# Kernel optimization log

Hardware: AMD Instinct MI355X
Metric: run time of the kernel (lower is better)

The kernel has to match this reference:

```python
import jax, jax.numpy as jnp
import numpy as np

N, E, F, R, L, B = 50000, 800000, 64, 20, 2, 64
RC = 5.0
ZMAX = 100
LN2 = 0.6931471805599453

def ssp(x):
    # shifted softplus: softplus(x) - log(2)
    return jax.nn.softplus(x) - LN2

def setup_inputs() -> dict:
    key = jax.random.key(0)
    ks = jax.random.split(key, 32)
    w = lambda i, shape: jax.random.normal(ks[i], shape, dtype=jnp.float32) * 0.05
    inp = {
        'z': jax.random.randint(ks[0], (N,), 0, ZMAX + 1),
        'pos': jax.random.normal(ks[1], (N, 3), dtype=jnp.float32) * 3.0,
        'edge_index': jax.random.randint(ks[2], (2, E), 0, N),
        'batch_idx': jnp.sort(jax.random.randint(ks[3], (N,), 0, B)),
        'emb': jax.random.normal(ks[4], (ZMAX + 1, F), dtype=jnp.float32),
        'phi_W': w(5, (L, 3 * F, F)), 'phi_b': w(6, (L, 3 * F)),
        'filt_W1': w(7, (L, F, R)), 'filt_b1': w(8, (L, F)),
        'filt_W2': w(9, (L, 3 * F, F)), 'filt_b2': w(10, (L, 3 * F)),
        'U_W': w(11, (L, F, F)), 'V_W': w(12, (L, F, F)),
        'a_W1': w(13, (L, F, 2 * F)), 'a_b1': w(14, (L, F)),
        'a_W2': w(15, (L, 3 * F, F)), 'a_b2': w(16, (L, 3 * F)),
        'e_W1': w(17, (F // 2, F)), 'e_b1': w(18, (F // 2,)),
        'e_W2': w(19, (1, F // 2)), 'e_b2': w(20, (1,)),
        'dip_w': w(21, (F,)),
    }
    return inp

def reference(z, pos, edge_index, batch_idx, emb, phi_W, phi_b,
              filt_W1, filt_b1, filt_W2, filt_b2, U_W, V_W,
              a_W1, a_b1, a_W2, a_b2, e_W1, e_b1, e_W2, e_b2, dip_w):
    src, dst = edge_index[0], edge_index[1]
    s = emb[z]                               # (N, F)
    v = jnp.zeros((N, F, 3), dtype=s.dtype)  # (N, F, 3)

    # edge geometry
    r_vec = pos[dst] - pos[src]              # (E, 3)
    r_norm = jnp.linalg.norm(r_vec, axis=-1)
    r_hat = r_vec / jnp.maximum(r_norm, 1e-8)[:, None]
    # Gaussian RBF on [0, RC], widths = grid spacing
    mu = jnp.linspace(0.0, RC, R, dtype=s.dtype)
    width = mu[1] - mu[0]
    e_ij = jnp.exp(-((r_norm[:, None] - mu[None, :]) ** 2) / (2.0 * width * width))
    fc = 0.5 * (jnp.cos(jnp.pi * r_norm / RC) + 1.0) * (r_norm < RC)
    e_ij = e_ij * fc[:, None]                # (E, R)

    for l in range(L):
        # message block
        filt = ssp(e_ij @ filt_W1[l].T + filt_b1[l]) @ filt_W2[l].T + filt_b2[l]  # (E, 3F)
        W_s, W_v, W_r = jnp.split(filt, 3, axis=-1)
        phi = s[dst] @ phi_W[l].T + phi_b[l]                                       # (E, 3F)
        phi_s, phi_v, phi_r = jnp.split(phi, 3, axis=-1)
        m_s = W_s * phi_s                                                          # (E, F)
        m_v = W_v[:, :, None] * v[dst] + (W_r * phi_r)[:, :, None] * r_hat[:, None, :]  # (E, F, 3)
        s = s + jax.ops.segment_sum(m_s, src, num_segments=N)
        v = v + jax.ops.segment_sum(m_v, src, num_segments=N)
        # update block
        Uv = jnp.einsum('nfd,gf->ngd', v, U_W[l])
        Vv = jnp.einsum('nfd,gf->ngd', v, V_W[l])
        Vv_norm_sq = jnp.sum(Vv * Vv, axis=-1)                                     # (N, F)
        a = ssp(jnp.concatenate([s, Vv_norm_sq], axis=-1) @ a_W1[l].T + a_b1[l]) @ a_W2[l].T + a_b2[l]
        a_ss, a_sv, a_vv = jnp.split(a, 3, axis=-1)
        inner = jnp.sum(Uv * Vv, axis=-1)
        s = s + a_ss + a_sv * inner
        v = v + a_vv[:, :, None] * Uv

    # heads
    eps_i = (ssp(s @ e_W1.T + e_b1) @ e_W2.T + e_b2)[:, 0]  # (N,)
    energy = jax.ops.segment_sum(eps_i, batch_idx, num_segments=B)
    mu_i = jnp.sum(v * dip_w[None, :, None], axis=1)         # (N, 3)
    mu_mol = jax.ops.segment_sum(mu_i, batch_idx, num_segments=B)
    dipole = jnp.linalg.norm(mu_mol, axis=-1)
    charges = jnp.zeros((N,), dtype=s.dtype)
    return energy, dipole, charges
```

## Files before the change

### kernel.cpp

```cpp
#include <hip/hip_runtime.h>
#include <math.h>

static constexpr int N  = 50000;
static constexpr int E  = 800000;
static constexpr int F  = 64;
static constexpr int R  = 20;
static constexpr int NL = 2;
static constexpr int B  = 64;
static constexpr float RC   = 5.0f;
static constexpr float LN2F = 0.6931471805599453f;
static constexpr float WIDTH  = RC / (R - 1);
static constexpr float INV2W2 = 1.0f / (2.0f * WIDTH * WIDTH);
static constexpr float PI_F = 3.14159265358979323846f;

static constexpr int   NB     = 4096;
static constexpr float DR     = RC / NB;
static constexpr float INV_DR = NB / RC;
static constexpr int   TROWS  = NB + 2;
static constexpr int   TENT   = NB + 1;

static constexpr int NBLK_SCAN = (N + 255) / 256;

typedef __attribute__((ext_vector_type(8))) short bf16x8;
typedef __attribute__((ext_vector_type(4))) float f32x4;

__device__ __forceinline__ float ssp_f(float x) {
    return fmaxf(x, 0.0f) + log1pf(__expf(-fabsf(x))) - LN2F;
}

__device__ __forceinline__ short f2bf(float x) {
    unsigned u = __builtin_bit_cast(unsigned, x);
    unsigned r = (u + 0x7fffu + ((u >> 16) & 1u)) >> 16;
    return (short)r;
}
__device__ __forceinline__ float bf_lo(unsigned u) {
    return __builtin_bit_cast(float, u << 16);
}
__device__ __forceinline__ float bf_hi(unsigned u) {
    return __builtin_bit_cast(float, u & 0xffff0000u);
}

__global__ void k_hist(const int* __restrict__ ei, int* __restrict__ cnt) {
    int e = blockIdx.x * blockDim.x + threadIdx.x;
    if (e < E) atomicAdd(&cnt[ei[e]], 1);
}

__global__ void k_scan_a(const int* __restrict__ cnt, int* __restrict__ bsum) {
    __shared__ int part[256];
    const int t = threadIdx.x;
    const int idx = blockIdx.x * 256 + t;
    int v = (idx < N) ? cnt[idx] : 0;
    part[t] = v;
    __syncthreads();
    for (int d = 1; d < 256; d <<= 1) {
        int x = (t >= d) ? part[t - d] : 0;
        __syncthreads();
        part[t] += x;
        __syncthreads();
    }
    if (t == 255) bsum[blockIdx.x] = part[255];
}

__global__ void k_scan_b(const int* __restrict__ bsum, int* __restrict__ bpre,
                         int* __restrict__ offN) {
    __shared__ int part[256];
    const int t = threadIdx.x;
    int v = (t < NBLK_SCAN) ? bsum[t] : 0;
    part[t] = v;
    __syncthreads();
    for (int d = 1; d < 256; d <<= 1) {
        int x = (t >= d) ? part[t - d] : 0;
        __syncthreads();
        part[t] += x;
        __syncthreads();
    }
    if (t < NBLK_SCAN) bpre[t] = part[t] - v;
    if (t == NBLK_SCAN - 1) *offN = part[t];
}

__global__ void k_scan_c(const int* __restrict__ cnt, const int* __restrict__ bpre,
                         int* __restrict__ off, int* __restrict__ cur) {
    __shared__ int part[256];
    const int t = threadIdx.x;
    const int idx = blockIdx.x * 256 + t;
    int v = (idx < N) ? cnt[idx] : 0;
    part[t] = v;
    __syncthreads();
    for (int d = 1; d < 256; d <<= 1) {
        int x = (t >= d) ? part[t - d] : 0;
        __syncthreads();
        part[t] += x;
        __syncthreads();
    }
    if (idx < N) {
        int e = bpre[blockIdx.x] + part[t] - v;
        off[idx] = e;
        cur[idx] = e;
    }
}

__global__ void k_scatter(const int* __restrict__ ei, int* __restrict__ cur,
                          const float* __restrict__ pos, uint4* __restrict__ edata) {
    int e = blockIdx.x * blockDim.x + threadIdx.x;
    if (e >= E) return;
    int src = ei[e], dst = ei[E + e];
    int p = atomicAdd(&cur[src], 1);
    float qx = pos[dst * 3 + 0] - pos[src * 3 + 0];
    float qy = pos[dst * 3 + 1] - pos[src * 3 + 1];
    float qz = pos[dst * 3 + 2] - pos[src * 3 + 2];
    float rn = sqrtf(qx * qx + qy * qy + qz * qz);
    float invn = 1.0f / fmaxf(rn, 1e-8f);
    float t = rn * INV_DR;
    int i = (int)t;
    float fr = t - (float)i;
    if (i >= NB) { i = NB; fr = 0.0f; }
    uint4 rec;
    rec.x = (unsigned)dst;
    rec.y = (unsigned)i | ((unsigned)(unsigned short)f2bf(fr) << 16);
    rec.z = (unsigned)(unsigned short)f2bf(qx * invn)
          | ((unsigned)(unsigned short)f2bf(qy * invn) << 16);
    rec.w = (unsigned)(unsigned short)f2bf(qz * invn);
    edata[p] = rec;
}

__global__ void k_table(const float* __restrict__ fW1, const float* __restrict__ fb1,
                        const float* __restrict__ fW2, const float* __restrict__ fb2,
                        unsigned short* __restrict__ Tp) {
    const int l   = blockIdx.x / TROWS;
    const int row = blockIdx.x % TROWS;
    const int lane = threadIdx.x;
    const float r = fminf((float)row, (float)NB) * DR;
    const float fc = (r < RC) ? 0.5f * (__cosf(PI_F * r * (1.0f / RC)) + 1.0f) : 0.0f;

    __shared__ float sh[F];
    float acc = fb1[l * F + lane];
    const float* w1 = fW1 + (size_t)l * F * R + (size_t)lane * R;
    #pragma unroll
    for (int rr = 0; rr < R; rr++) {
        float dmu = r - rr * WIDTH;
        float er = __expf(-dmu * dmu * INV2W2) * fc;
        acc = fmaf(er, w1[rr], acc);
    }
    sh[lane] = ssp_f(acc);
    __syncthreads();
    unsigned short* TpL = Tp + (size_t)l * TENT * 384;
    #pragma unroll
    for (int p = 0; p < 3; p++) {
        int c = p * 64 + lane;
        float a = fb2[l * 192 + c];
        const float* w2 = fW2 + ((size_t)l * 192 + c) * 64;
        #pragma unroll 8
        for (int k = 0; k < F; k++) a = fmaf(sh[k], w2[k], a);
        unsigned short bf = (unsigned short)f2bf(a);
        if (row <= NB) TpL[(size_t)row * 384 + c * 2 + 0] = bf;
        if (row >= 1)  TpL[(size_t)(row - 1) * 384 + c * 2 + 1] = bf;
    }
}

template<bool HASV>
__launch_bounds__(256)
__global__ void k_pack(float* __restrict__ s, const float* __restrict__ v,
                       const int* __restrict__ z, const float* __restrict__ emb,
                       const float* __restrict__ PW, const float* __restrict__ Pb,
                       unsigned short* __restrict__ nd) {
    __shared__ float sbuf[4][F];
    const int lane = threadIdx.x & 63;
    const int wid  = threadIdx.x >> 6;
    const int gwave = blockIdx.x * 4 + wid;
    const int nwaves = gridDim.x * 4;

    float ws[F], wr[F];
    {
        const float* rs = PW + (size_t)lane * 64;
        const float* rr = PW + (size_t)(128 + lane) * 64;
        #pragma unroll
        for (int k = 0; k < F; k += 4) {
            float4 a = *(const float4*)(rs + k);
            ws[k] = a.x; ws[k+1] = a.y; ws[k+2] = a.z; ws[k+3] = a.w;
            float4 b = *(const float4*)(rr + k);
            wr[k] = b.x; wr[k+1] = b.y; wr[k+2] = b.z; wr[k+3] = b.w;
        }
    }
    const float bs = Pb[lane], br = Pb[128 + lane];

    for (int n = gwave; n < N; n += nwaves) {
        float sv;
        if (HASV) {
            sv = s[(size_t)n * F + lane];
        } else {
            sv = emb[(size_t)z[n] * F + lane];
            s[(size_t)n * F + lane] = sv;
        }
        sbuf[wid][lane] = sv;
        float as = bs, ar = br;
        #pragma unroll
        for (int k = 0; k < F; k += 4) {
            float4 s4 = *(const float4*)&sbuf[wid][k];
            as = fmaf(s4.x, ws[k],   as); as = fmaf(s4.y, ws[k+1], as);
            as = fmaf(s4.z, ws[k+2], as); as = fmaf(s4.w, ws[k+3], as);
            ar = fmaf(s4.x, wr[k],   ar); ar = fmaf(s4.y, wr[k+1], ar);
            ar = fmaf(s4.z, wr[k+2], ar); ar = fmaf(s4.w, wr[k+3], ar);
        }
        unsigned short* rec = nd + (size_t)n * 320;
        rec[lane]      = (unsigned short)f2bf(as);
        rec[64 + lane] = (unsigned short)f2bf(ar);
        if (HASV) {
            #pragma unroll
            for (int d = 0; d < 3; d++)
                rec[128 + d * 64 + lane] =
                    (unsigned short)f2bf(v[((size_t)n * 3 + d) * F + lane]);
        }
    }
}

template<bool ACCUMV>
__launch_bounds__(256)
__global__ void k_gather(const uint4* __restrict__ edata, const int* __restrict__ off,
                         const unsigned short* __restrict__ TpL,
                         const unsigned short* __restrict__ nd,
                         float* __restrict__ s, float* __restrict__ v) {
    const int lane = threadIdx.x & 63;
    const int wid  = threadIdx.x >> 6;
    const int n = blockIdx.x * 4 + wid;
    if (n >= N) return;
    const int base = off[n], end = off[n + 1];
    float ms = 0.f, mv0 = 0.f, mv1 = 0.f, mv2 = 0.f;

    for (int k = base; k < end; ++k) {
        const uint4 ed = edata[k];
        const int dst = (int)ed.x;
        const int   i  = (int)(ed.y & 0xffffu);
        const float fr = bf_hi(ed.y);
        const float rhx = bf_lo(ed.z), rhy = bf_hi(ed.z), rhz = bf_lo(ed.w);

        const unsigned* tp = (const unsigned*)(TpL + (size_t)i * 384);
        const unsigned us = tp[lane];
        const unsigned ur = tp[128 + lane];
        const float Ws = fmaf(fr, bf_hi(us) - bf_lo(us), bf_lo(us));
        const float Wr = fmaf(fr, bf_hi(ur) - bf_lo(ur), bf_lo(ur));

        const unsigned short* rec = nd + (size_t)dst * 320;
        const float ps = bf_lo((unsigned)rec[lane]);
        const float pr = bf_lo((unsigned)rec[64 + lane]);
        ms = fmaf(Ws, ps, ms);
        const float c = Wr * pr;
        if (ACCUMV) {
            const unsigned uv = tp[64 + lane];
            const float Wv = fmaf(fr, bf_hi(uv) - bf_lo(uv), bf_lo(uv));
            const float v0 = bf_lo((unsigned)rec[128 + lane]);
            const float v1 = bf_lo((unsigned)rec[192 + lane]);
            const float v2 = bf_lo((unsigned)rec[256 + lane]);
            mv0 = fmaf(Wv, v0, fmaf(c, rhx, mv0));
            mv1 = fmaf(Wv, v1, fmaf(c, rhy, mv1));
            mv2 = fmaf(Wv, v2, fmaf(c, rhz, mv2));
        } else {
            mv0 = fmaf(c, rhx, mv0);
            mv1 = fmaf(c, rhy, mv1);
            mv2 = fmaf(c, rhz, mv2);
        }
    }
    s[(size_t)n * F + lane] += ms;
    float* vo = v + (size_t)n * 3 * F + lane;
    if (ACCUMV) {
        vo[0]     += mv0;
        vo[F]     += mv1;
        vo[2 * F] += mv2;
    } else {
        vo[0] = mv0; vo[F] = mv1; vo[2 * F] = mv2;
    }
}

__device__ __forceinline__ bf16x8 load_wfrag(const float* __restrict__ Wp, int ldk,
                                             int nrow, int k0) {
    const float* p = Wp + (size_t)nrow * ldk + k0;
    float4 a = *(const float4*)p;
    float4 b = *(const float4*)(p + 4);
    bf16x8 r;
    r[0] = f2bf(a.x); r[1] = f2bf(a.y); r[2] = f2bf(a.z); r[3] = f2bf(a.w);
    r[4] = f2bf(b.x); r[5] = f2bf(b.y); r[6] = f2bf(b.z); r[7] = f2bf(b.w);
    return r;
}

__launch_bounds__(256)
__global__ void k_update_mfma(float* __restrict__ s, float* __restrict__ v,
                              const float* __restrict__ U_W, const float* __restrict__ V_W,
                              const float* __restrict__ aW1, const float* __restrict__ ab1,
                              const float* __restrict__ aW2, const float* __restrict__ ab2) {
    __shared__ short vlds[96 * 72];
    __shared__ short xlds[32 * 136];
    __shared__ short hlds[32 * 72];

    const int tid = threadIdx.x;
    const int l   = tid & 63;
    const int w   = tid >> 6;
    const int lo  = l & 15;
    const int hi  = l >> 4;

    bf16x8 ufr[2], vfr[2], w1fr[4], w2fr[3][2];
    #pragma unroll
    for (int kk = 0; kk < 2; kk++) {
        ufr[kk] = load_wfrag(U_W, 64, w * 16 + lo, kk * 32 + hi * 8);
        vfr[kk] = load_wfrag(V_W, 64, w * 16 + lo, kk * 32 + hi * 8);
    }
    #pragma unroll
    for (int kk = 0; kk < 4; kk++)
        w1fr[kk] = load_wfrag(aW1, 128, w * 16 + lo, kk * 32 + hi * 8);
    #pragma unroll
    for (int p = 0; p < 3; p++)
        #pragma unroll
        for (int kk = 0; kk < 2; kk++)
            w2fr[p][kk] = load_wfrag(aW2, 64, p * 64 + w * 16 + lo, kk * 32 + hi * 8);

    const float ab1c  = ab1[w * 16 + lo];
    const float ab2c0 = ab2[w * 16 + lo];
    const float ab2c1 = ab2[64 + w * 16 + lo];
    const float ab2c2 = ab2[128 + w * 16 + lo];
    const int g = w * 16 + lo;

    for (int half = 0; half < 2; half++) {
        const int n0 = blockIdx.x * 64 + half * 32;
        if (half) __syncthreads();

        for (int u = tid; u < 96 * 8; u += 256) {
            int row = u >> 3, oct = u & 7;
            int d = row >> 5, nn = row & 31;
            int n = min(n0 + nn, N - 1);
            const float* src = v + ((size_t)n * 3 + d) * 64 + oct * 8;
            float4 a = *(const float4*)src;
            float4 b = *(const float4*)(src + 4);
            bf16x8 t;
            t[0] = f2bf(a.x); t[1] = f2bf(a.y); t[2] = f2bf(a.z); t[3] = f2bf(a.w);
            t[4] = f2bf(b.x); t[5] = f2bf(b.y); t[6] = f2bf(b.z); t[7] = f2bf(b.w);
            *(bf16x8*)&vlds[row * 72 + oct * 8] = t;
        }
        for (int u = tid; u < 32 * 8; u += 256) {
            int nn = u >> 3, oct = u & 7;
            int n = min(n0 + nn, N - 1);
            const float* src = s + (size_t)n * 64 + oct * 8;
            float4 a = *(const float4*)src;
            float4 b = *(const float4*)(src + 4);
            bf16x8 t;
            t[0] = f2bf(a.x); t[1] = f2bf(a.y); t[2] = f2bf(a.z); t[3] = f2bf(a.w);
            t[4] = f2bf(b.x); t[5] = f2bf(b.y); t[6] = f2bf(b.z); t[7] = f2bf(b.w);
            *(bf16x8*)&xlds[nn * 136 + oct * 8] = t;
        }
        __syncthreads();

        f32x4 cu[6], cv[6];
        #pragma unroll
        for (int mt = 0; mt < 6; mt++) { cu[mt] = (f32x4)0.0f; cv[mt] = (f32x4)0.0f; }
        #pragma unroll
        for (int kk = 0; kk < 2; kk++) {
            #pragma unroll
            for (int mt = 0; mt < 6; mt++) {
                bf16x8 af = *(const bf16x8*)&vlds[(mt * 16 + lo) * 72 + kk * 32 + hi * 8];
                cu[mt] = __builtin_amdgcn_mfma_f32_16x16x32_bf16(af, ufr[kk], cu[mt], 0, 0, 0);
                cv[mt] = __builtin_amdgcn_mfma_f32_16x16x32_bf16(af, vfr[kk], cv[mt], 0, 0, 0);
            }
        }

        f32x4 inn[2];
        #pragma unroll
        for (int nt = 0; nt < 2; nt++) {
            #pragma unroll
            for (int r = 0; r < 4; r++) {
                float vs = 0.f, ii = 0.f;
                #pragma unroll
                for (int d = 0; d < 3; d++) {
                    float a = cu[d * 2 + nt][r], b = cv[d * 2 + nt][r];
                    vs = fmaf(b, b, vs);
                    ii = fmaf(a, b, ii);
                }
                inn[nt][r] = ii;
                int nl = nt * 16 + hi * 4 + r;
                xlds[nl * 136 + 64 + w * 16 + lo] = f2bf(vs);
            }
        }
        __syncthreads();

        f32x4 c2[2];
        c2[0] = (f32x4)0.0f; c2[1] = (f32x4)0.0f;
        #pragma unroll
        for (int kk = 0; kk < 4; kk++) {
            #pragma unroll
            for (int mt = 0; mt < 2; mt++) {
                bf16x8 af = *(const bf16x8*)&xlds[(mt * 16 + lo) * 136 + kk * 32 + hi * 8];
                c2[mt] = __builtin_amdgcn_mfma_f32_16x16x32_bf16(af, w1fr[kk], c2[mt], 0, 0, 0);
            }
        }
        #pragma unroll
        for (int mt = 0; mt < 2; mt++)
            #pragma unroll
            for (int r = 0; r < 4; r++) {
                float hv = ssp_f(c2[mt][r] + ab1c);
                hlds[(mt * 16 + hi * 4 + r) * 72 + w * 16 + lo] = f2bf(hv);
            }
        __syncthreads();

        f32x4 c3[2][3];
        #pragma unroll
        for (int mt = 0; mt < 2; mt++)
            #pragma unroll
            for (int p = 0; p < 3; p++) c3[mt][p] = (f32x4)0.0f;
        #pragma unroll
        for (int kk = 0; kk < 2; kk++) {
            #pragma unroll
            for (int mt = 0; mt < 2; mt++) {
                bf16x8 af = *(const bf16x8*)&hlds[(mt * 16 + lo) * 72 + kk * 32 + hi * 8];
                #pragma unroll
                for (int p = 0; p < 3; p++)
                    c3[mt][p] = __builtin_amdgcn_mfma_f32_16x16x32_bf16(af, w2fr[p][kk], c3[mt][p], 0, 0, 0);
            }
        }

        #pragma unroll
        for (int mt = 0; mt < 2; mt++) {
            #pragma unroll
            for (int r = 0; r < 4; r++) {
                int n = n0 + mt * 16 + hi * 4 + r;
                if (n >= N) continue;
                float a_ss = c3[mt][0][r] + ab2c0;
                float a_sv = c3[mt][1][r] + ab2c1;
                float a_vv = c3[mt][2][r] + ab2c2;
                size_t si = (size_t)n * 64 + g;
                s[si] = s[si] + a_ss + a_sv * inn[mt][r];
                #pragma unroll
                for (int d = 0; d < 3; d++) {
                    size_t vi = ((size_t)n * 3 + d) * 64 + g;
                    v[vi] = v[vi] + a_vv * cu[d * 2 + mt][r];
                }
            }
        }
    }
}

__global__ void k_heads(const float* __restrict__ s, const float* __restrict__ v,
                        const int* __restrict__ batch_idx,
                        const float* __restrict__ eW1, const float* __restrict__ eb1,
                        const float* __restrict__ eW2, const float* __restrict__ eb2,
                        const float* __restrict__ dip_w,
                        float* __restrict__ eacc, float* __restrict__ macc) {
    __shared__ float se[B];
    __shared__ float sm[3][B];
    if (threadIdx.x < B) se[threadIdx.x] = 0.0f;
    if (threadIdx.x < 3 * B) sm[threadIdx.x >> 6][threadIdx.x & 63] = 0.0f;
    __syncthreads();
    int n = blockIdx.x * blockDim.x + threadIdx.x;
    if (n < N) {
        int b = batch_idx[n];
        float sr[F];
        #pragma unroll
        for (int f = 0; f < F; f += 4) {
            float4 t = *(const float4*)&s[(size_t)n * F + f];
            sr[f] = t.x; sr[f+1] = t.y; sr[f+2] = t.z; sr[f+3] = t.w;
        }
        float eps = eb2[0];
        for (int jj = 0; jj < F / 2; jj++) {
            float acc = eb1[jj];
            #pragma unroll
            for (int f = 0; f < F; f++)
                acc = fmaf(sr[f], eW1[jj * F + f], acc);
            eps = fmaf(eW2[jj], ssp_f(acc), eps);
        }
        atomicAdd(&se[b], eps);
        #pragma unroll
        for (int d = 0; d < 3; d++) {
            float m = 0.0f;
            #pragma unroll 8
            for (int f = 0; f < F; f++)
                m = fmaf(v[((size_t)n * 3 + d) * F + f], dip_w[f], m);
            atomicAdd(&sm[d][b], m);
        }
    }
    __syncthreads();
    if (threadIdx.x < B) atomicAdd(&eacc[threadIdx.x], se[threadIdx.x]);
    if (threadIdx.x >= B && threadIdx.x < 4 * B) {
        int d = (threadIdx.x >> 6) - 1, b = threadIdx.x & 63;
        atomicAdd(&macc[d * B + b], sm[d][b]);
    }
}

__global__ void k_final(const float* __restrict__ eacc, const float* __restrict__ macc,
                        float* __restrict__ out) {
    int b = threadIdx.x;
    if (b < B) {
        out[b] = eacc[b];
        float mx = macc[b], my = macc[B + b], mz = macc[2 * B + b];
        out[B + b] = sqrtf(mx * mx + my * my + mz * mz);
    }
}

extern "C" void kernel_launch(void* const* d_in, const int* in_sizes, int n_in,
                              void* d_out, int out_size, void* d_ws, size_t ws_size,
                              hipStream_t stream) {
    const int*   z     = (const int*)d_in[0];
    const float* pos   = (const float*)d_in[1];
    const int*   ei    = (const int*)d_in[2];
    const int*   bidx  = (const int*)d_in[3];
    const float* emb   = (const float*)d_in[4];
    const float* phi_W = (const float*)d_in[5];
    const float* phi_b = (const float*)d_in[6];
    const float* fW1   = (const float*)d_in[7];
    const float* fb1   = (const float*)d_in[8];
    const float* fW2   = (const float*)d_in[9];
    const float* fb2   = (const float*)d_in[10];
    const float* U_W   = (const float*)d_in[11];
    const float* V_W   = (const float*)d_in[12];
    const float* aW1   = (const float*)d_in[13];
    const float* ab1   = (const float*)d_in[14];
    const float* aW2   = (const float*)d_in[15];
    const float* ab2   = (const float*)d_in[16];
    const float* eW1   = (const float*)d_in[17];
    const float* eb1   = (const float*)d_in[18];
    const float* eW2   = (const float*)d_in[19];
    const float* eb2   = (const float*)d_in[20];
    const float* dip_w = (const float*)d_in[21];
    float* out = (float*)d_out;

    float* ws = (float*)d_ws;
    float* s    = ws;
    float* v    = s + (size_t)N * F;
    unsigned short* nd = (unsigned short*)(v + (size_t)N * F * 3);
    unsigned short* Tp = nd + (size_t)N * 320;
    float* eacc = (float*)(Tp + (size_t)NL * TENT * 384);
    float* macc = eacc + B;
    int*   cnt  = (int*)(macc + 3 * B);
    int*   off  = cnt  + N;
    int*   cur  = off  + N + 1;
    int*   bsum = cur  + N;
    int*   bpre = bsum + 256;
    uint4* edata = (uint4*)(((uintptr_t)(bpre + 256) + 15) & ~(uintptr_t)15);

    hipMemsetAsync(cnt,  0, sizeof(int) * N, stream);
    hipMemsetAsync(eacc, 0, sizeof(float) * 4 * B, stream);
    hipMemsetAsync(out + 2 * B, 0, sizeof(float) * (size_t)N, stream);

    k_hist<<<(E + 255) / 256, 256, 0, stream>>>(ei, cnt);
    k_scan_a<<<NBLK_SCAN, 256, 0, stream>>>(cnt, bsum);
    k_scan_b<<<1, 256, 0, stream>>>(bsum, bpre, off + N);
    k_scan_c<<<NBLK_SCAN, 256, 0, stream>>>(cnt, bpre, off, cur);
    k_scatter<<<(E + 255) / 256, 256, 0, stream>>>(ei, cur, pos, edata);
    k_table<<<NL * TROWS, 64, 0, stream>>>(fW1, fb1, fW2, fb2, Tp);

    const int gblocks = (N + 3) / 4;
    const int ublocks = (N + 63) / 64;
    k_pack<false><<<512, 256, 0, stream>>>(s, nullptr, z, emb, phi_W, phi_b, nd);
    k_gather<false><<<gblocks, 256, 0, stream>>>(edata, off, Tp, nd, s, v);
    k_update_mfma<<<ublocks, 256, 0, stream>>>(s, v,
        U_W, V_W, aW1, ab1, aW2, ab2);
    k_pack<true><<<512, 256, 0, stream>>>(s, v, z, emb, phi_W + (size_t)192 * 64,
                                          phi_b + 192, nd);
    k_gather<true><<<gblocks, 256, 0, stream>>>(edata, off,
        Tp + (size_t)TENT * 384, nd, s, v);
    k_update_mfma<<<ublocks, 256, 0, stream>>>(s, v,
        U_W + 4096, V_W + 4096, aW1 + 8192, ab1 + F, aW2 + 12288, ab2 + 192);

    k_heads<<<(N + 255) / 256, 256, 0, stream>>>(s, v, bidx, eW1, eb1, eW2, eb2,
                                                 dip_w, eacc, macc);
    k_final<<<1, 64, 0, stream>>>(eacc, macc, out);
}
```

Baseline: 535.3 us.

## Fuse layer-2 node packing into update kernel and interleave gather table layout

Removes the separate pack kernel for layer 2 by computing the phi projections with MFMA inside the first update kernel, which writes the packed bf16 node records directly. The filter table becomes lane-interleaved, so each lane fetches its Ws/Wv/Wr interpolation pairs with one 16-byte load. Node data is split into a packed s-projection array and a packed v array, making gather loads single dword or uint2 per lane. The gather loop is unrolled by two with independent accumulators to expose more memory-level parallelism. This adds LDS syncs and MFMA work to the update kernel and enlarges the table by a third with padding.

```diff
diff --git a/kernel.cpp b/kernel.cpp
--- a/kernel.cpp
+++ b/kernel.cpp
@@ -143,7 +143,7 @@
     }
     sh[lane] = ssp_f(acc);
     __syncthreads();
-    unsigned short* TpL = Tp + (size_t)l * TENT * 384;
+    unsigned short* TpL = Tp + (size_t)l * TENT * 512;
     #pragma unroll
     for (int p = 0; p < 3; p++) {
         int c = p * 64 + lane;
@@ -152,64 +152,83 @@
         #pragma unroll 8
         for (int k = 0; k < F; k++) a = fmaf(sh[k], w2[k], a);
         unsigned short bf = (unsigned short)f2bf(a);
-        if (row <= NB) TpL[(size_t)row * 384 + c * 2 + 0] = bf;
-        if (row >= 1)  TpL[(size_t)(row - 1) * 384 + c * 2 + 1] = bf;
-    }
-}
-
-template<bool HASV>
+        if (row <= NB) TpL[(size_t)row * 512 + lane * 8 + p * 2 + 0] = bf;
+        if (row >= 1)  TpL[(size_t)(row - 1) * 512 + lane * 8 + p * 2 + 1] = bf;
+    }
+    if (row <= NB) {
+        TpL[(size_t)row * 512 + lane * 8 + 6] = 0;
+        TpL[(size_t)row * 512 + lane * 8 + 7] = 0;
+    }
+}
+
 __launch_bounds__(256)
-__global__ void k_pack(float* __restrict__ s, const float* __restrict__ v,
-                       const int* __restrict__ z, const float* __restrict__ emb,
-                       const float* __restrict__ PW, const float* __restrict__ Pb,
-                       unsigned short* __restrict__ nd) {
+__global__ void k_pack0(float* __restrict__ s, const int* __restrict__ z,
+                        const float* __restrict__ emb,
+                        const float* __restrict__ PW, const float* __restrict__ Pb,
+                        unsigned* __restrict__ ndA) {
     __shared__ float sbuf[4][F];
     const int lane = threadIdx.x & 63;
     const int wid  = threadIdx.x >> 6;
     const int gwave = blockIdx.x * 4 + wid;
     const int nwaves = gridDim.x * 4;
 
-    float ws[F], wr[F];
+    float wsr[F], wrr[F];
     {
         const float* rs = PW + (size_t)lane * 64;
         const float* rr = PW + (size_t)(128 + lane) * 64;
         #pragma unroll
         for (int k = 0; k < F; k += 4) {
             float4 a = *(const float4*)(rs + k);
-            ws[k] = a.x; ws[k+1] = a.y; ws[k+2] = a.z; ws[k+3] = a.w;
+            wsr[k] = a.x; wsr[k+1] = a.y; wsr[k+2] = a.z; wsr[k+3] = a.w;
             float4 b = *(const float4*)(rr + k);
-            wr[k] = b.x; wr[k+1] = b.y; wr[k+2] = b.z; wr[k+3] = b.w;
+            wrr[k] = b.x; wrr[k+1] = b.y; wrr[k+2] = b.z; wrr[k+3] = b.w;
         }
     }
     const float bs = Pb[lane], br = Pb[128 + lane];
 
     for (int n = gwave; n < N; n += nwaves) {
-        float sv;
-        if (HASV) {
-            sv = s[(size_t)n * F + lane];
-        } else {
-            sv = emb[(size_t)z[n] * F + lane];
-            s[(size_t)n * F + lane] = sv;
-        }
+        float sv = emb[(size_t)z[n] * F + lane];
+        s[(size_t)n * F + lane] = sv;
         sbuf[wid][lane] = sv;
         float as = bs, ar = br;
         #pragma unroll
         for (int k = 0; k < F; k += 4) {
             float4 s4 = *(const float4*)&sbuf[wid][k];
-            as = fmaf(s4.x, ws[k],   as); as = fmaf(s4.y, ws[k+1], as);
-            as = fmaf(s4.z, ws[k+2], as); as = fmaf(s4.w, ws[k+3], as);
-            ar = fmaf(s4.x, wr[k],   ar); ar = fmaf(s4.y, wr[k+1], ar);
-            ar = fmaf(s4.z, wr[k+2], ar); ar = fmaf(s4.w, wr[k+3], ar);
-        }
-        unsigned short* rec = nd + (size_t)n * 320;
-        rec[lane]      = (unsigned short)f2bf(as);
-        rec[64 + lane] = (unsigned short)f2bf(ar);
-        if (HASV) {
-            #pragma unroll
-            for (int d = 0; d < 3; d++)
-                rec[128 + d * 64 + lane] =
-                    (unsigned short)f2bf(v[((size_t)n * 3 + d) * F + lane]);
-        }
+            as = fmaf(s4.x, wsr[k],   as); as = fmaf(s4.y, wsr[k+1], as);
+            as = fmaf(s4.z, wsr[k+2], as); as = fmaf(s4.w, wsr[k+3], as);
+            ar = fmaf(s4.x, wrr[k],   ar); ar = fmaf(s4.y, wrr[k+1], ar);
+            ar = fmaf(s4.z, wrr[k+2], ar); ar = fmaf(s4.w, wrr[k+3], ar);
+        }
+        ndA[(size_t)n * 64 + lane] = (unsigned)(unsigned short)f2bf(as)
+                                   | ((unsigned)(unsigned short)f2bf(ar) << 16);
+    }
+}
+
+template<bool ACCUMV>
+__device__ __forceinline__ void edge_step(const uint4 ed,
+                                          const unsigned short* __restrict__ TpL,
+                                          const unsigned* __restrict__ ndA,
+                                          const uint2* __restrict__ ndV, int lane,
+                                          float& ms, float& mv0, float& mv1, float& mv2) {
+    const int   i  = (int)(ed.y & 0xffffu);
+    const float fr = bf_hi(ed.y);
+    const uint4 t  = *(const uint4*)(TpL + (size_t)i * 512 + lane * 8);
+    const unsigned a = ndA[(size_t)ed.x * 64 + lane];
+    const float Ws = fmaf(fr, bf_hi(t.x) - bf_lo(t.x), bf_lo(t.x));
+    const float Wr = fmaf(fr, bf_hi(t.z) - bf_lo(t.z), bf_lo(t.z));
+    ms = fmaf(Ws, bf_lo(a), ms);
+    const float c = Wr * bf_hi(a);
+    const float rhx = bf_lo(ed.z), rhy = bf_hi(ed.z), rhz = bf_lo(ed.w);
+    if (ACCUMV) {
+        const float Wv = fmaf(fr, bf_hi(t.y) - bf_lo(t.y), bf_lo(t.y));
+        const uint2 w = ndV[(size_t)ed.x * 64 + lane];
+        mv0 = fmaf(Wv, bf_lo(w.x), fmaf(c, rhx, mv0));
+        mv1 = fmaf(Wv, bf_hi(w.x), fmaf(c, rhy, mv1));
+        mv2 = fmaf(Wv, bf_lo(w.y), fmaf(c, rhz, mv2));
+    } else {
+        mv0 = fmaf(c, rhx, mv0);
+        mv1 = fmaf(c, rhy, mv1);
+        mv2 = fmaf(c, rhz, mv2);
     }
 }
 
@@ -217,48 +236,30 @@
 __launch_bounds__(256)
 __global__ void k_gather(const uint4* __restrict__ edata, const int* __restrict__ off,
                          const unsigned short* __restrict__ TpL,
-                         const unsigned short* __restrict__ nd,
+                         const unsigned* __restrict__ ndA, const uint2* __restrict__ ndV,
                          float* __restrict__ s, float* __restrict__ v) {
     const int lane = threadIdx.x & 63;
     const int wid  = threadIdx.x >> 6;
     const int n = blockIdx.x * 4 + wid;
     if (n >= N) return;
     const int base = off[n], end = off[n + 1];
-    float ms = 0.f, mv0 = 0.f, mv1 = 0.f, mv2 = 0.f;
-
-    for (int k = base; k < end; ++k) {
-        const uint4 ed = edata[k];
-        const int dst = (int)ed.x;
-        const int   i  = (int)(ed.y & 0xffffu);
-        const float fr = bf_hi(ed.y);
-        const float rhx = bf_lo(ed.z), rhy = bf_hi(ed.z), rhz = bf_lo(ed.w);
-
-        const unsigned* tp = (const unsigned*)(TpL + (size_t)i * 384);
-        const unsigned us = tp[lane];
-        const unsigned ur = tp[128 + lane];
-        const float Ws = fmaf(fr, bf_hi(us) - bf_lo(us), bf_lo(us));
-        const float Wr = fmaf(fr, bf_hi(ur) - bf_lo(ur), bf_lo(ur));
-
-        const unsigned short* rec = nd + (size_t)dst * 320;
-        const float ps = bf_lo((unsigned)rec[lane]);
-        const float pr = bf_lo((unsigned)rec[64 + lane]);
-        ms = fmaf(Ws, ps, ms);
-        const float c = Wr * pr;
-        if (ACCUMV) {
-            const unsigned uv = tp[64 + lane];
-            const float Wv = fmaf(fr, bf_hi(uv) - bf_lo(uv), bf_lo(uv));
-            const float v0 = bf_lo((unsigned)rec[128 + lane]);
-            const float v1 = bf_lo((unsigned)rec[192 + lane]);
-            const float v2 = bf_lo((unsigned)rec[256 + lane]);
-            mv0 = fmaf(Wv, v0, fmaf(c, rhx, mv0));
-            mv1 = fmaf(Wv, v1, fmaf(c, rhy, mv1));
-            mv2 = fmaf(Wv, v2, fmaf(c, rhz, mv2));
-        } else {
-            mv0 = fmaf(c, rhx, mv0);
-            mv1 = fmaf(c, rhy, mv1);
-            mv2 = fmaf(c, rhz, mv2);
-        }
-    }
+    float msA = 0.f, a0 = 0.f, a1 = 0.f, a2 = 0.f;
+    float msB = 0.f, b0 = 0.f, b1 = 0.f, b2 = 0.f;
+
+    int k = base;
+    for (; k + 1 < end; k += 2) {
+        const uint4 e0 = edata[k];
+        const uint4 e1 = edata[k + 1];
+        edge_step<ACCUMV>(e0, TpL, ndA, ndV, lane, msA, a0, a1, a2);
+        edge_step<ACCUMV>(e1, TpL, ndA, ndV, lane, msB, b0, b1, b2);
+    }
+    if (k < end) {
+        const uint4 e0 = edata[k];
+        edge_step<ACCUMV>(e0, TpL, ndA, ndV, lane, msA, a0, a1, a2);
+    }
+    const float ms = msA + msB;
+    const float mv0 = a0 + b0, mv1 = a1 + b1, mv2 = a2 + b2;
+
     s[(size_t)n * F + lane] += ms;
     float* vo = v + (size_t)n * 3 * F + lane;
     if (ACCUMV) {
@@ -281,11 +282,14 @@
     return r;
 }
 
+template<bool DO_PACK>
 __launch_bounds__(256)
 __global__ void k_update_mfma(float* __restrict__ s, float* __restrict__ v,
                               const float* __restrict__ U_W, const float* __restrict__ V_W,
                               const float* __restrict__ aW1, const float* __restrict__ ab1,
-                              const float* __restrict__ aW2, const float* __restrict__ ab2) {
+                              const float* __restrict__ aW2, const float* __restrict__ ab2,
+                              const float* __restrict__ PW, const float* __restrict__ Pb,
+                              unsigned* __restrict__ ndA, uint2* __restrict__ ndV) {
     __shared__ short vlds[96 * 72];
     __shared__ short xlds[32 * 136];
     __shared__ short hlds[32 * 72];
@@ -310,6 +314,18 @@
         #pragma unroll
         for (int kk = 0; kk < 2; kk++)
             w2fr[p][kk] = load_wfrag(aW2, 64, p * 64 + w * 16 + lo, kk * 32 + hi * 8);
+
+    bf16x8 pws[2], pwr[2];
+    float pbs = 0.f, pbr = 0.f;
+    if (DO_PACK) {
+        #pragma unroll
+        for (int kk = 0; kk < 2; kk++) {
+            pws[kk] = load_wfrag(PW, 64, w * 16 + lo, kk * 32 + hi * 8);
+            pwr[kk] = load_wfrag(PW, 64, 128 + w * 16 + lo, kk * 32 + hi * 8);
+        }
+        pbs = Pb[w * 16 + lo];
+        pbr = Pb[128 + w * 16 + lo];
+    }
 
     const float ab1c  = ab1[w * 16 + lo];
     const float ab2c0 = ab2[w * 16 + lo];
@@ -413,21 +429,67 @@
             }
         }
 
+        float snew[2][4];
         #pragma unroll
         for (int mt = 0; mt < 2; mt++) {
             #pragma unroll
             for (int r = 0; r < 4; r++) {
                 int n = n0 + mt * 16 + hi * 4 + r;
-                if (n >= N) continue;
+                if (n >= N) { snew[mt][r] = 0.f; continue; }
                 float a_ss = c3[mt][0][r] + ab2c0;
                 float a_sv = c3[mt][1][r] + ab2c1;
                 float a_vv = c3[mt][2][r] + ab2c2;
                 size_t si = (size_t)n * 64 + g;
-                s[si] = s[si] + a_ss + a_sv * inn[mt][r];
+                float sn = s[si] + a_ss + a_sv * inn[mt][r];
+                s[si] = sn;
+                snew[mt][r] = sn;
+                float vn[3];
                 #pragma unroll
                 for (int d = 0; d < 3; d++) {
                     size_t vi = ((size_t)n * 3 + d) * 64 + g;
-                    v[vi] = v[vi] + a_vv * cu[d * 2 + mt][r];
+                    vn[d] = v[vi] + a_vv * cu[d * 2 + mt][r];
+                    v[vi] = vn[d];
+                }
+                if (DO_PACK) {
+                    uint2 pv;
+                    pv.x = (unsigned)(unsigned short)f2bf(vn[0])
+                         | ((unsigned)(unsigned short)f2bf(vn[1]) << 16);
+                    pv.y = (unsigned)(unsigned short)f2bf(vn[2]);
+                    ndV[(size_t)n * 64 + g] = pv;
+                }
+            }
+        }
+
+        if (DO_PACK) {
+            __syncthreads();
+            #pragma unroll
+            for (int mt = 0; mt < 2; mt++)
+                #pragma unroll
+                for (int r = 0; r < 4; r++)
+                    hlds[(mt * 16 + hi * 4 + r) * 72 + g] = f2bf(snew[mt][r]);
+            __syncthreads();
+
+            f32x4 cs[2], cr[2];
+            cs[0] = (f32x4)0.0f; cs[1] = (f32x4)0.0f;
+            cr[0] = (f32x4)0.0f; cr[1] = (f32x4)0.0f;
+            #pragma unroll
+            for (int kk = 0; kk < 2; kk++) {
+                #pragma unroll
+                for (int mt = 0; mt < 2; mt++) {
+                    bf16x8 af = *(const bf16x8*)&hlds[(mt * 16 + lo) * 72 + kk * 32 + hi * 8];
+                    cs[mt] = __builtin_amdgcn_mfma_f32_16x16x32_bf16(af, pws[kk], cs[mt], 0, 0, 0);
+                    cr[mt] = __builtin_amdgcn_mfma_f32_16x16x32_bf16(af, pwr[kk], cr[mt], 0, 0, 0);
+                }
+            }
+            #pragma unroll
+            for (int mt = 0; mt < 2; mt++) {
+                #pragma unroll
+                for (int r = 0; r < 4; r++) {
+                    int n = n0 + mt * 16 + hi * 4 + r;
+                    if (n >= N) continue;
+                    ndA[(size_t)n * 64 + g] =
+                          (unsigned)(unsigned short)f2bf(cs[mt][r] + pbs)
+                        | ((unsigned)(unsigned short)f2bf(cr[mt][r] + pbr) << 16);
                 }
             }
         }
@@ -520,9 +582,10 @@
     float* ws = (float*)d_ws;
     float* s    = ws;
     float* v    = s + (size_t)N * F;
-    unsigned short* nd = (unsigned short*)(v + (size_t)N * F * 3);
-    unsigned short* Tp = nd + (size_t)N * 320;
-    float* eacc = (float*)(Tp + (size_t)NL * TENT * 384);
+    unsigned* ndA = (unsigned*)(v + (size_t)N * F * 3);
+    uint2* ndV  = (uint2*)(ndA + (size_t)N * 64);
+    unsigned short* Tp = (unsigned short*)(ndV + (size_t)N * 64);
+    float* eacc = (float*)(Tp + (size_t)NL * TENT * 512);
     float* macc = eacc + B;
     int*   cnt  = (int*)(macc + 3 * B);
     int*   off  = cnt  + N;
@@ -544,16 +607,16 @@
 
     const int gblocks = (N + 3) / 4;
     const int ublocks = (N + 63) / 64;
-    k_pack<false><<<512, 256, 0, stream>>>(s, nullptr, z, emb, phi_W, phi_b, nd);
-    k_gather<false><<<gblocks, 256, 0, stream>>>(edata, off, Tp, nd, s, v);
-    k_update_mfma<<<ublocks, 256, 0, stream>>>(s, v,
-        U_W, V_W, aW1, ab1, aW2, ab2);
-    k_pack<true><<<512, 256, 0, stream>>>(s, v, z, emb, phi_W + (size_t)192 * 64,
-                                          phi_b + 192, nd);
+    k_pack0<<<512, 256, 0, stream>>>(s, z, emb, phi_W, phi_b, ndA);
+    k_gather<false><<<gblocks, 256, 0, stream>>>(edata, off, Tp, ndA, ndV, s, v);
+    k_update_mfma<true><<<ublocks, 256, 0, stream>>>(s, v,
+        U_W, V_W, aW1, ab1, aW2, ab2,
+        phi_W + (size_t)192 * 64, phi_b + 192, ndA, ndV);
     k_gather<true><<<gblocks, 256, 0, stream>>>(edata, off,
-        Tp + (size_t)TENT * 384, nd, s, v);
-    k_update_mfma<<<ublocks, 256, 0, stream>>>(s, v,
-        U_W + 4096, V_W + 4096, aW1 + 8192, ab1 + F, aW2 + 12288, ab2 + 192);
+        Tp + (size_t)TENT * 512, ndA, ndV, s, v);
+    k_update_mfma<false><<<ublocks, 256, 0, stream>>>(s, v,
+        U_W + 4096, V_W + 4096, aW1 + 8192, ab1 + F, aW2 + 12288, ab2 + 192,
+        nullptr, nullptr, nullptr, nullptr);
 
     k_heads<<<(N + 255) / 256, 256, 0, stream>>>(s, v, bidx, eW1, eb1, eW2, eb2,
                                                  dip_w, eacc, macc);
```

After: 562.1 us. 1.05x slower.
